# Kernel optimization log

Measured on AMD Instinct MI355X. Metric: run time of the kernel, lower is better.

The kernel has to match this reference:

```python
import jax, jax.numpy as jnp
import numpy as np

B = 524288
HIDDEN = 128
EXP_MAX = 88.0

def setup_inputs() -> dict:
    key = jax.random.key(0)
    ks = jax.random.split(key, 5)
    t = jax.random.uniform(ks[0], (B,), dtype=jnp.float32)
    u = jax.random.uniform(ks[1], (B, 10), dtype=jnp.float32)
    p = jax.random.uniform(ks[2], (37,), dtype=jnp.float32)
    W1 = jax.random.normal(ks[3], (5, HIDDEN), dtype=jnp.float32) * 0.1
    b1 = jnp.zeros((HIDDEN,), jnp.float32)
    W2 = jax.random.normal(ks[4], (HIDDEN, 2), dtype=jnp.float32) * 0.1
    b2 = jnp.zeros((2,), jnp.float32)
    return {"t": t, "u": u, "p": p, "W1": W1, "b1": b1, "W2": W2, "b2": b2}

def reference(t, u, p, W1, b1, W2, b2):
    # state unpack: u[:, i] are per-instance scalars, shape [B]
    Qmt, Qav, Qtc, Qpv, Vlv, Vao, Vvc, Vrv, Vpa, Vpu = (u[:, i] for i in range(10))
    (Elvf, Eao, Evc, Ervf, Epa, Epu, Rmt, Rav, Rsys, Rtc, Rpv, Rpul,
     Lmt, Lav, Ltc, Lpv, Vdlvf, Vdao, Vdvc, Vdrvf, Vdpa, Vdpu,
     P0lvf, P0rvf, lamlvf, lamrvf, Espt, V0lvf, V0rvf, P0spt, P0pcd,
     V0spt, V0pcd, lamspt, lampcd, Vdspt, Pth) = (p[i] for i in range(37))

    # cardiac driver function
    e = jnp.exp(-80.0 * (jnp.mod(t, 0.75) - 0.375) ** 2)

    # small surrogate MLP: [B,5] -> [B,2] (tanh hidden)
    inp = jnp.stack([Vlv, Vao, Vvc, Vrv, Vpa], axis=-1)
    h = jnp.tanh(inp @ W1 + b1)
    z = h @ W2 + b2
    Pperi, Vspt = z[:, 0], z[:, 1]

    Vlvf = Vlv - Vspt
    Vrvf = Vrv + Vspt
    exp_lv = jnp.exp(jnp.minimum(lamlvf * (Vlvf - V0lvf), EXP_MAX))
    exp_rv = jnp.exp(jnp.minimum(lamrvf * (Vrvf - V0rvf), EXP_MAX))

    Plvf = e * Elvf * (Vlvf - Vdlvf) + (1.0 - e) * P0lvf * (exp_lv - 1.0)
    Prvf = e * Ervf * (Vrvf - Vdrvf) + (1.0 - e) * P0rvf * (exp_rv - 1.0)
    Plv = Plvf + Pperi
    Prv = Prvf + Pperi
    Pao = Eao * (Vao - Vdao)
    Pvc = Evc * (Vvc - Vdvc)
    Ppa = Epa * (Vpa - Vdpa) + Pth
    Ppu = Epu * (Vpu - Vdpu) + Pth
    Qsys = (Pao - Pvc) / Rsys
    Qpul = (Ppa - Ppu) / Rpul

    # valve flows with open/closed branching (computed with un-clamped Q)
    du0 = jnp.where((Ppu - Plv > 0) | (Qmt > 0), (Ppu - Plv - Qmt * Rmt) / Lmt, 0.0)
    du1 = jnp.where((Plv - Pao > 0) | (Qav > 0), (Plv - Pao - Qav * Rav) / Lav, 0.0)
    du2 = jnp.where((Pvc - Prv > 0) | (Qtc > 0), (Pvc - Prv - Qtc * Rtc) / Ltc, 0.0)
    du3 = jnp.where((Prv - Ppa > 0) | (Qpv > 0), (Prv - Ppa - Qpv * Rpv) / Lpv, 0.0)

    # volumes use clamped (non-negative) flows
    Qmt_c = jnp.maximum(Qmt, 0.0)
    Qav_c = jnp.maximum(Qav, 0.0)
    Qtc_c = jnp.maximum(Qtc, 0.0)
    Qpv_c = jnp.maximum(Qpv, 0.0)
    du4 = Qmt_c - Qav_c
    du5 = Qav_c - Qsys
    du6 = Qsys - Qtc_c
    du7 = Qtc_c - Qpv_c
    du8 = Qpv_c - Qpul
    du9 = Qpul - Qmt_c

    return jnp.stack([du0, du1, du2, du3, du4, du5, du6, du7, du8, du9], axis=-1)
```

## Files before the change

### kernel.cpp

```cpp
#include <hip/hip_runtime.h>

#define B_TOTAL 524288
#define HID 128

__global__ __launch_bounds__(256, 8) void ode_kernel(
    const float* __restrict__ t,
    const float* __restrict__ u,
    const float* __restrict__ p,
    const float* __restrict__ W1,
    const float* __restrict__ b1,
    const float* __restrict__ W2,
    const float* __restrict__ b2,
    float* __restrict__ out)
{
    __shared__ float wpk[HID * 8];
    const int tid = threadIdx.x;
    for (int j = tid; j < HID; j += 256) {
        wpk[j * 8 + 0] = W1[0 * HID + j];
        wpk[j * 8 + 1] = W1[1 * HID + j];
        wpk[j * 8 + 2] = W1[2 * HID + j];
        wpk[j * 8 + 3] = W1[3 * HID + j];
        wpk[j * 8 + 4] = W1[4 * HID + j];
        wpk[j * 8 + 5] = b1[j];
        wpk[j * 8 + 6] = W2[j * 2 + 0];
        wpk[j * 8 + 7] = W2[j * 2 + 1];
    }
    __syncthreads();

    const int row = blockIdx.x * 256 + tid;

    const float2* u2 = reinterpret_cast<const float2*>(u + (size_t)row * 10);
    float2 ua = u2[0], ub = u2[1], uc = u2[2], ud = u2[3], ue = u2[4];
    const float Qmt = ua.x, Qav = ua.y, Qtc = ub.x, Qpv = ub.y;
    const float Vlv = uc.x, Vao = uc.y, Vvc = ud.x, Vrv = ud.y;
    const float Vpa = ue.x, Vpu = ue.y;

    const float tv = t[row];
    const float m  = (tv >= 0.75f) ? (tv - 0.75f) : tv;
    const float dd = m - 0.375f;
    const float e  = __expf(-80.0f * dd * dd);

    float z0 = b2[0], z1 = b2[1];
#pragma unroll 4
    for (int j = 0; j < HID; ++j) {
        const float* w = &wpk[j * 8];
        float a = w[5];
        a = fmaf(Vlv, w[0], a);
        a = fmaf(Vao, w[1], a);
        a = fmaf(Vvc, w[2], a);
        a = fmaf(Vrv, w[3], a);
        a = fmaf(Vpa, w[4], a);
        const float e2 = __expf(2.0f * a);
        const float th = 1.0f - 2.0f * __builtin_amdgcn_rcpf(e2 + 1.0f);
        z0 = fmaf(th, w[6], z0);
        z1 = fmaf(th, w[7], z1);
    }
    const float Pperi = z0, Vspt = z1;

    const float Elvf = p[0],  Eao = p[1],   Evc = p[2],   Ervf = p[3];
    const float Epa  = p[4],  Epu = p[5];
    const float Rmt  = p[6],  Rav = p[7],   Rsys = p[8],  Rtc = p[9];
    const float Rpv  = p[10], Rpul = p[11];
    const float Lmt  = p[12], Lav = p[13],  Ltc = p[14],  Lpv = p[15];
    const float Vdlvf = p[16], Vdao = p[17], Vdvc = p[18], Vdrvf = p[19];
    const float Vdpa  = p[20], Vdpu = p[21];
    const float P0lvf = p[22], P0rvf = p[23];
    const float lamlvf = p[24], lamrvf = p[25];
    const float V0lvf = p[27], V0rvf = p[28];
    const float Pth   = p[36];

    const float Vlvf = Vlv - Vspt;
    const float Vrvf = Vrv + Vspt;
    const float alv = fminf(lamlvf * (Vlvf - V0lvf), 88.0f);
    const float arv = fminf(lamrvf * (Vrvf - V0rvf), 88.0f);
    const float exp_lv = __expf(alv);
    const float exp_rv = __expf(arv);
    const float ome = 1.0f - e;
    const float Plvf = e * Elvf * (Vlvf - Vdlvf) + ome * P0lvf * (exp_lv - 1.0f);
    const float Prvf = e * Ervf * (Vrvf - Vdrvf) + ome * P0rvf * (exp_rv - 1.0f);
    const float Plv = Plvf + Pperi;
    const float Prv = Prvf + Pperi;
    const float Pao = Eao * (Vao - Vdao);
    const float Pvc = Evc * (Vvc - Vdvc);
    const float Ppa = fmaf(Epa, Vpa - Vdpa, Pth);
    const float Ppu = fmaf(Epu, Vpu - Vdpu, Pth);
    const float Qsys = (Pao - Pvc) / Rsys;
    const float Qpul = (Ppa - Ppu) / Rpul;

    const float du0 = ((Ppu - Plv > 0.0f) || (Qmt > 0.0f)) ? (Ppu - Plv - Qmt * Rmt) / Lmt : 0.0f;
    const float du1 = ((Plv - Pao > 0.0f) || (Qav > 0.0f)) ? (Plv - Pao - Qav * Rav) / Lav : 0.0f;
    const float du2 = ((Pvc - Prv > 0.0f) || (Qtc > 0.0f)) ? (Pvc - Prv - Qtc * Rtc) / Ltc : 0.0f;
    const float du3 = ((Prv - Ppa > 0.0f) || (Qpv > 0.0f)) ? (Prv - Ppa - Qpv * Rpv) / Lpv : 0.0f;

    const float Qmt_c = fmaxf(Qmt, 0.0f);
    const float Qav_c = fmaxf(Qav, 0.0f);
    const float Qtc_c = fmaxf(Qtc, 0.0f);
    const float Qpv_c = fmaxf(Qpv, 0.0f);
    const float du4 = Qmt_c - Qav_c;
    const float du5 = Qav_c - Qsys;
    const float du6 = Qsys - Qtc_c;
    const float du7 = Qtc_c - Qpv_c;
    const float du8 = Qpv_c - Qpul;
    const float du9 = Qpul - Qmt_c;

    float2* o2 = reinterpret_cast<float2*>(out + (size_t)row * 10);
    o2[0] = make_float2(du0, du1);
    o2[1] = make_float2(du2, du3);
    o2[2] = make_float2(du4, du5);
    o2[3] = make_float2(du6, du7);
    o2[4] = make_float2(du8, du9);
}

extern "C" void kernel_launch(void* const* d_in, const int* in_sizes, int n_in,
                              void* d_out, int out_size, void* d_ws, size_t ws_size,
                              hipStream_t stream) {
    const float* t  = (const float*)d_in[0];
    const float* u  = (const float*)d_in[1];
    const float* p  = (const float*)d_in[2];
    const float* W1 = (const float*)d_in[3];
    const float* b1 = (const float*)d_in[4];
    const float* W2 = (const float*)d_in[5];
    const float* b2 = (const float*)d_in[6];
    float* out = (float*)d_out;

    dim3 grid(B_TOTAL / 256), block(256);
    ode_kernel<<<grid, block, 0, stream>>>(t, u, p, W1, b1, W2, b2, out);
}
```

Before: 107.9 us.

## Process four rows per thread with prepacked prescaled weights and exp2 math

A separate tiny kernel prepacks W1, b1 and W2 into a workspace buffer, with the first layer prescaled by 2*log2(e) so the tanh can use the raw v_exp_f32 (exp2) instruction directly. The main kernel drops the per-block shared-memory staging and barrier, and each thread now handles four rows, reading each weight once per four rows through float4 global/scalar loads. Row I/O uses float4 vectors, and the divisions by parameters become reciprocal multiplies. The cost is much higher register pressure, a quarter as many threads (launch bounds lowered to 2), an extra kernel launch, and small precision differences from the reciprocal and exp2 approximations.

```diff
diff --git a/kernel.cpp b/kernel.cpp
--- a/kernel.cpp
+++ b/kernel.cpp
@@ -2,60 +2,74 @@
 
 #define B_TOTAL 524288
 #define HID 128
+#define ROWS 4
+#define BLK 256
+#define NBLK (B_TOTAL / ROWS / BLK)
 
-__global__ __launch_bounds__(256, 8) void ode_kernel(
+static __device__ __forceinline__ float fast_exp2(float x) {
+    float r;
+    asm("v_exp_f32 %0, %1" : "=v"(r) : "v"(x));
+    return r;
+}
+
+__global__ void pack_w(const float* __restrict__ W1, const float* __restrict__ b1,
+                       const float* __restrict__ W2, float* __restrict__ wp) {
+    const int j = threadIdx.x;
+    if (j < HID) {
+        const float s = 2.8853900817779268f;
+        wp[j * 8 + 0] = W1[0 * HID + j] * s;
+        wp[j * 8 + 1] = W1[1 * HID + j] * s;
+        wp[j * 8 + 2] = W1[2 * HID + j] * s;
+        wp[j * 8 + 3] = W1[3 * HID + j] * s;
+        wp[j * 8 + 4] = W1[4 * HID + j] * s;
+        wp[j * 8 + 5] = b1[j] * s;
+        wp[j * 8 + 6] = W2[j * 2 + 0];
+        wp[j * 8 + 7] = W2[j * 2 + 1];
+    }
+}
+
+__global__ __launch_bounds__(BLK, 2) void ode_kernel(
     const float* __restrict__ t,
     const float* __restrict__ u,
     const float* __restrict__ p,
-    const float* __restrict__ W1,
-    const float* __restrict__ b1,
-    const float* __restrict__ W2,
+    const float* __restrict__ wp,
     const float* __restrict__ b2,
     float* __restrict__ out)
 {
-    __shared__ float wpk[HID * 8];
-    const int tid = threadIdx.x;
-    for (int j = tid; j < HID; j += 256) {
-        wpk[j * 8 + 0] = W1[0 * HID + j];
-        wpk[j * 8 + 1] = W1[1 * HID + j];
-        wpk[j * 8 + 2] = W1[2 * HID + j];
-        wpk[j * 8 + 3] = W1[3 * HID + j];
-        wpk[j * 8 + 4] = W1[4 * HID + j];
-        wpk[j * 8 + 5] = b1[j];
-        wpk[j * 8 + 6] = W2[j * 2 + 0];
-        wpk[j * 8 + 7] = W2[j * 2 + 1];
-    }
-    __syncthreads();
+    const int g = blockIdx.x * BLK + threadIdx.x;
 
-    const int row = blockIdx.x * 256 + tid;
+    float ub[ROWS * 10];
+    const float4* u4 = reinterpret_cast<const float4*>(u + (size_t)g * (ROWS * 10));
+#pragma unroll
+    for (int i = 0; i < 10; ++i) reinterpret_cast<float4*>(ub)[i] = u4[i];
 
-    const float2* u2 = reinterpret_cast<const float2*>(u + (size_t)row * 10);
-    float2 ua = u2[0], ub = u2[1], uc = u2[2], ud = u2[3], ue = u2[4];
-    const float Qmt = ua.x, Qav = ua.y, Qtc = ub.x, Qpv = ub.y;
-    const float Vlv = uc.x, Vao = uc.y, Vvc = ud.x, Vrv = ud.y;
-    const float Vpa = ue.x, Vpu = ue.y;
+    const float4 tv4 = *reinterpret_cast<const float4*>(t + (size_t)g * ROWS);
+    const float tv[ROWS] = {tv4.x, tv4.y, tv4.z, tv4.w};
 
-    const float tv = t[row];
-    const float m  = (tv >= 0.75f) ? (tv - 0.75f) : tv;
-    const float dd = m - 0.375f;
-    const float e  = __expf(-80.0f * dd * dd);
+    const float b20 = b2[0], b21 = b2[1];
+    float z0[ROWS], z1[ROWS];
+#pragma unroll
+    for (int r = 0; r < ROWS; ++r) { z0[r] = b20; z1[r] = b21; }
 
-    float z0 = b2[0], z1 = b2[1];
+    const float4* wp4 = reinterpret_cast<const float4*>(wp);
 #pragma unroll 4
     for (int j = 0; j < HID; ++j) {
-        const float* w = &wpk[j * 8];
-        float a = w[5];
-        a = fmaf(Vlv, w[0], a);
-        a = fmaf(Vao, w[1], a);
-        a = fmaf(Vvc, w[2], a);
-        a = fmaf(Vrv, w[3], a);
-        a = fmaf(Vpa, w[4], a);
-        const float e2 = __expf(2.0f * a);
-        const float th = 1.0f - 2.0f * __builtin_amdgcn_rcpf(e2 + 1.0f);
-        z0 = fmaf(th, w[6], z0);
-        z1 = fmaf(th, w[7], z1);
+        const float4 wa = wp4[2 * j];
+        const float4 wb = wp4[2 * j + 1];
+#pragma unroll
+        for (int r = 0; r < ROWS; ++r) {
+            float y = wb.y;
+            y = fmaf(ub[r * 10 + 4], wa.x, y);
+            y = fmaf(ub[r * 10 + 5], wa.y, y);
+            y = fmaf(ub[r * 10 + 6], wa.z, y);
+            y = fmaf(ub[r * 10 + 7], wa.w, y);
+            y = fmaf(ub[r * 10 + 8], wb.x, y);
+            const float e2 = fast_exp2(y);
+            const float th = 1.0f - 2.0f * __builtin_amdgcn_rcpf(e2 + 1.0f);
+            z0[r] = fmaf(th, wb.z, z0[r]);
+            z1[r] = fmaf(th, wb.w, z1[r]);
+        }
     }
-    const float Pperi = z0, Vspt = z1;
 
     const float Elvf = p[0],  Eao = p[1],   Evc = p[2],   Ervf = p[3];
     const float Epa  = p[4],  Epu = p[5];
@@ -69,46 +83,67 @@
     const float V0lvf = p[27], V0rvf = p[28];
     const float Pth   = p[36];
 
-    const float Vlvf = Vlv - Vspt;
-    const float Vrvf = Vrv + Vspt;
-    const float alv = fminf(lamlvf * (Vlvf - V0lvf), 88.0f);
-    const float arv = fminf(lamrvf * (Vrvf - V0rvf), 88.0f);
-    const float exp_lv = __expf(alv);
-    const float exp_rv = __expf(arv);
-    const float ome = 1.0f - e;
-    const float Plvf = e * Elvf * (Vlvf - Vdlvf) + ome * P0lvf * (exp_lv - 1.0f);
-    const float Prvf = e * Ervf * (Vrvf - Vdrvf) + ome * P0rvf * (exp_rv - 1.0f);
-    const float Plv = Plvf + Pperi;
-    const float Prv = Prvf + Pperi;
-    const float Pao = Eao * (Vao - Vdao);
-    const float Pvc = Evc * (Vvc - Vdvc);
-    const float Ppa = fmaf(Epa, Vpa - Vdpa, Pth);
-    const float Ppu = fmaf(Epu, Vpu - Vdpu, Pth);
-    const float Qsys = (Pao - Pvc) / Rsys;
-    const float Qpul = (Ppa - Ppu) / Rpul;
+    const float L2E = 1.4426950408889634f;
+    const float inv_Rsys = __builtin_amdgcn_rcpf(Rsys);
+    const float inv_Rpul = __builtin_amdgcn_rcpf(Rpul);
+    const float inv_Lmt  = __builtin_amdgcn_rcpf(Lmt);
+    const float inv_Lav  = __builtin_amdgcn_rcpf(Lav);
+    const float inv_Ltc  = __builtin_amdgcn_rcpf(Ltc);
+    const float inv_Lpv  = __builtin_amdgcn_rcpf(Lpv);
+    const float laml_l2e = lamlvf * L2E;
+    const float lamr_l2e = lamrvf * L2E;
+    const float CLAMP2 = 88.0f * L2E;
 
-    const float du0 = ((Ppu - Plv > 0.0f) || (Qmt > 0.0f)) ? (Ppu - Plv - Qmt * Rmt) / Lmt : 0.0f;
-    const float du1 = ((Plv - Pao > 0.0f) || (Qav > 0.0f)) ? (Plv - Pao - Qav * Rav) / Lav : 0.0f;
-    const float du2 = ((Pvc - Prv > 0.0f) || (Qtc > 0.0f)) ? (Pvc - Prv - Qtc * Rtc) / Ltc : 0.0f;
-    const float du3 = ((Prv - Ppa > 0.0f) || (Qpv > 0.0f)) ? (Prv - Ppa - Qpv * Rpv) / Lpv : 0.0f;
+    float du[ROWS * 10];
+#pragma unroll
+    for (int r = 0; r < ROWS; ++r) {
+        const float Qmt = ub[r * 10 + 0], Qav = ub[r * 10 + 1];
+        const float Qtc = ub[r * 10 + 2], Qpv = ub[r * 10 + 3];
+        const float Vlv = ub[r * 10 + 4], Vao = ub[r * 10 + 5];
+        const float Vvc = ub[r * 10 + 6], Vrv = ub[r * 10 + 7];
+        const float Vpa = ub[r * 10 + 8], Vpu = ub[r * 10 + 9];
+        const float Pperi = z0[r], Vspt = z1[r];
 
-    const float Qmt_c = fmaxf(Qmt, 0.0f);
-    const float Qav_c = fmaxf(Qav, 0.0f);
-    const float Qtc_c = fmaxf(Qtc, 0.0f);
-    const float Qpv_c = fmaxf(Qpv, 0.0f);
-    const float du4 = Qmt_c - Qav_c;
-    const float du5 = Qav_c - Qsys;
-    const float du6 = Qsys - Qtc_c;
-    const float du7 = Qtc_c - Qpv_c;
-    const float du8 = Qpv_c - Qpul;
-    const float du9 = Qpul - Qmt_c;
+        const float m  = (tv[r] >= 0.75f) ? (tv[r] - 0.75f) : tv[r];
+        const float dd = m - 0.375f;
+        const float e  = fast_exp2(dd * dd * (-80.0f * L2E));
 
-    float2* o2 = reinterpret_cast<float2*>(out + (size_t)row * 10);
-    o2[0] = make_float2(du0, du1);
-    o2[1] = make_float2(du2, du3);
-    o2[2] = make_float2(du4, du5);
-    o2[3] = make_float2(du6, du7);
-    o2[4] = make_float2(du8, du9);
+        const float Vlvf = Vlv - Vspt;
+        const float Vrvf = Vrv + Vspt;
+        const float exp_lv = fast_exp2(fminf(laml_l2e * (Vlvf - V0lvf), CLAMP2));
+        const float exp_rv = fast_exp2(fminf(lamr_l2e * (Vrvf - V0rvf), CLAMP2));
+        const float ome = 1.0f - e;
+        const float Plvf = e * Elvf * (Vlvf - Vdlvf) + ome * P0lvf * (exp_lv - 1.0f);
+        const float Prvf = e * Ervf * (Vrvf - Vdrvf) + ome * P0rvf * (exp_rv - 1.0f);
+        const float Plv = Plvf + Pperi;
+        const float Prv = Prvf + Pperi;
+        const float Pao = Eao * (Vao - Vdao);
+        const float Pvc = Evc * (Vvc - Vdvc);
+        const float Ppa = fmaf(Epa, Vpa - Vdpa, Pth);
+        const float Ppu = fmaf(Epu, Vpu - Vdpu, Pth);
+        const float Qsys = (Pao - Pvc) * inv_Rsys;
+        const float Qpul = (Ppa - Ppu) * inv_Rpul;
+
+        du[r * 10 + 0] = ((Ppu - Plv > 0.0f) || (Qmt > 0.0f)) ? (Ppu - Plv - Qmt * Rmt) * inv_Lmt : 0.0f;
+        du[r * 10 + 1] = ((Plv - Pao > 0.0f) || (Qav > 0.0f)) ? (Plv - Pao - Qav * Rav) * inv_Lav : 0.0f;
+        du[r * 10 + 2] = ((Pvc - Prv > 0.0f) || (Qtc > 0.0f)) ? (Pvc - Prv - Qtc * Rtc) * inv_Ltc : 0.0f;
+        du[r * 10 + 3] = ((Prv - Ppa > 0.0f) || (Qpv > 0.0f)) ? (Prv - Ppa - Qpv * Rpv) * inv_Lpv : 0.0f;
+
+        const float Qmt_c = fmaxf(Qmt, 0.0f);
+        const float Qav_c = fmaxf(Qav, 0.0f);
+        const float Qtc_c = fmaxf(Qtc, 0.0f);
+        const float Qpv_c = fmaxf(Qpv, 0.0f);
+        du[r * 10 + 4] = Qmt_c - Qav_c;
+        du[r * 10 + 5] = Qav_c - Qsys;
+        du[r * 10 + 6] = Qsys - Qtc_c;
+        du[r * 10 + 7] = Qtc_c - Qpv_c;
+        du[r * 10 + 8] = Qpv_c - Qpul;
+        du[r * 10 + 9] = Qpul - Qmt_c;
+    }
+
+    float4* o4 = reinterpret_cast<float4*>(out + (size_t)g * (ROWS * 10));
+#pragma unroll
+    for (int i = 0; i < 10; ++i) o4[i] = reinterpret_cast<const float4*>(du)[i];
 }
 
 extern "C" void kernel_launch(void* const* d_in, const int* in_sizes, int n_in,
@@ -122,7 +157,8 @@
     const float* W2 = (const float*)d_in[5];
     const float* b2 = (const float*)d_in[6];
     float* out = (float*)d_out;
+    float* wp  = (float*)d_ws;
 
-    dim3 grid(B_TOTAL / 256), block(256);
-    ode_kernel<<<grid, block, 0, stream>>>(t, u, p, W1, b1, W2, b2, out);
+    pack_w<<<1, HID, 0, stream>>>(W1, b1, W2, wp);
+    ode_kernel<<<NBLK, BLK, 0, stream>>>(t, u, p, wp, b2, out);
 }
```

After: 111.0 us. +2.9%, slower.
